# Optimization experiments

Measured on AMD Instinct MI355X. Metric: run time of the kernel, lower is better.

## Reference

```python
import jax, jax.numpy as jnp
import numpy as np

B, S, D, H, F = 2, 2048, 3072, 32, 8192
DH = D // H  # 96
EPS = 1e-5


def setup_inputs() -> dict:
    key = jax.random.key(0)
    ks = jax.random.split(key, 16)
    sd = 0.02
    inp = {
        "hidden_states": jax.random.normal(ks[0], (B, S, D), jnp.float32),
        "ln1_g": jnp.ones((D,), jnp.float32),
        "ln1_b": jnp.zeros((D,), jnp.float32),
        "Wq": jax.random.normal(ks[1], (D, H, DH), jnp.float32) * sd,
        "bq": jnp.zeros((H, DH), jnp.float32),
        "Wk": jax.random.normal(ks[2], (D, H, DH), jnp.float32) * sd,
        "bk": jnp.zeros((H, DH), jnp.float32),
        "Wv": jax.random.normal(ks[3], (D, H, DH), jnp.float32) * sd,
        "bv": jnp.zeros((H, DH), jnp.float32),
        "Wo": jax.random.normal(ks[4], (H, DH, D), jnp.float32) * sd,
        "bo": jnp.zeros((D,), jnp.float32),
        "ln2_g": jnp.ones((D,), jnp.float32),
        "ln2_b": jnp.zeros((D,), jnp.float32),
        "W1": jax.random.normal(ks[5], (D, F), jnp.float32) * sd,
        "b1": jnp.zeros((F,), jnp.float32),
        "W2": jax.random.normal(ks[6], (F, D), jnp.float32) * sd,
        "b2": jnp.zeros((D,), jnp.float32),
    }
    return inp


def _layernorm(x, g, b):
    m = jnp.mean(x, axis=-1, keepdims=True)
    v = jnp.mean(jnp.square(x - m), axis=-1, keepdims=True)
    return (x - m) * jax.lax.rsqrt(v + EPS) * g + b


def reference(hidden_states, ln1_g, ln1_b, Wq, bq, Wk, bk, Wv, bv, Wo, bo,
              ln2_g, ln2_b, W1, b1, W2, b2):
    # --- LN + self-attention + residual ---
    h = _layernorm(hidden_states, ln1_g, ln1_b)  # [B,S,D]
    q = jnp.einsum('bsd,dhk->bshk', h, Wq) + bq  # [B,S,H,DH]
    k = jnp.einsum('bsd,dhk->bshk', h, Wk) + bk
    v = jnp.einsum('bsd,dhk->bshk', h, Wv) + bv
    scale = 1.0 / np.sqrt(DH).astype(np.float32)
    scores = jnp.einsum('bshk,bthk->bhst', q, k) * scale  # [B,H,S,S]
    attn = jax.nn.softmax(scores, axis=-1)
    ctx = jnp.einsum('bhst,bthk->bshk', attn, v)  # [B,S,H,DH]
    attn_out = jnp.einsum('bshk,hkd->bsd', ctx, Wo) + bo
    h1 = hidden_states + attn_out
    # --- LN + MLP + residual ---
    h2 = _layernorm(h1, ln2_g, ln2_b)
    mlp = jax.nn.gelu(h2 @ W1 + b1, approximate=False) @ W2 + b2
    return h1 + mlp
```

## Files before the change

### kernel.cpp

```cpp
#include <hip/hip_runtime.h>
#include <math.h>

#define DEV __device__ __forceinline__

typedef __attribute__((ext_vector_type(8))) __bf16 bfrag;
typedef __attribute__((ext_vector_type(4))) float f4;
typedef __attribute__((ext_vector_type(8))) unsigned short u16x8;
typedef __attribute__((ext_vector_type(4))) unsigned short u16x4;

DEV unsigned short f2bf(float f) {
  unsigned u = __float_as_uint(f);
  u += 0x7fff + ((u >> 16) & 1);
  return (unsigned short)(u >> 16);
}

DEV void gload_lds16(const void* g, void* l) {
  __builtin_amdgcn_global_load_lds((const __attribute__((address_space(1))) void*)g,
                                   (__attribute__((address_space(3))) void*)l, 16, 0, 0);
}

template<int EPI, int OUTBF, int BIASROW>
__global__ __launch_bounds__(256, 2)
void gemm_bt(const unsigned short* __restrict__ A,
             const unsigned short* __restrict__ Bt,
             const float* __restrict__ bias,
             const float* __restrict__ res,
             void* __restrict__ outp,
             int M, int N, int K, int gm, int cm, int cn)
{
  __shared__ unsigned short As[2][128 * 32];
  __shared__ unsigned short Bs[2][128 * 32];
  const int tid = threadIdx.x;
  const int lane = tid & 63;
  const int wid = tid >> 6;
  const int wr = wid >> 1, wc = wid & 1;
  const int l15 = lane & 15, lg = lane >> 4;

  const int xcd = blockIdx.x & 7, bidx = blockIdx.x >> 3;
  const int cgm = gm / cm;
  const int tm = (xcd % cgm) * cm + bidx % cm;
  const int tn = (xcd / cgm) * cn + bidx / cm;
  const long tM = (long)tm * 128;
  const long tN = (long)tn * 128;

  const int c0 = tid, c1 = tid + 256;
  const int r0 = c0 >> 2, k0 = (c0 & 3) * 8;
  const int r1 = c1 >> 2, k1 = (c1 & 3) * 8;

  const unsigned short* A0 = A + (tM + r0) * (long)K + k0;
  const unsigned short* A1 = A + (tM + r1) * (long)K + k1;
  const unsigned short* B0 = Bt + (tN + r0) * (long)K + k0;
  const unsigned short* B1 = Bt + (tN + r1) * (long)K + k1;

  auto stage = [&](int kt, int buf) {
    const long ko = (long)kt * 32;
    gload_lds16(A0 + ko, &As[buf][c0 * 8]);
    gload_lds16(A1 + ko, &As[buf][c1 * 8]);
    gload_lds16(B0 + ko, &Bs[buf][c0 * 8]);
    gload_lds16(B1 + ko, &Bs[buf][c1 * 8]);
  };

  stage(0, 0);
  f4 acc[4][4] = {};
  const int nk = K >> 5;
  int cur = 0;
  __syncthreads();
  for (int kt = 0; kt < nk; ++kt) {
    if (kt + 1 < nk) stage(kt + 1, cur ^ 1);
    bfrag aF[4], bF[4];
#pragma unroll
    for (int m = 0; m < 4; ++m)
      aF[m] = *(const bfrag*)&As[cur][(wr * 64 + m * 16 + l15) * 32 + lg * 8];
#pragma unroll
    for (int n = 0; n < 4; ++n)
      bF[n] = *(const bfrag*)&Bs[cur][(wc * 64 + n * 16 + l15) * 32 + lg * 8];
#pragma unroll
    for (int m = 0; m < 4; ++m)
#pragma unroll
      for (int n = 0; n < 4; ++n)
        acc[m][n] = __builtin_amdgcn_mfma_f32_16x16x32_bf16(aF[m], bF[n], acc[m][n], 0, 0, 0);
    __syncthreads();
    cur ^= 1;
  }

#pragma unroll
  for (int m = 0; m < 4; ++m) {
#pragma unroll
    for (int n = 0; n < 4; ++n) {
      const long col = tN + wc * 64 + n * 16 + l15;
      const float bcol = BIASROW ? 0.f : bias[col];
#pragma unroll
      for (int e = 0; e < 4; ++e) {
        const long row = tM + wr * 64 + m * 16 + lg * 4 + e;
        float v = acc[m][n][e] + (BIASROW ? bias[row] : bcol);
        if constexpr (EPI == 1) v = 0.5f * v * (1.0f + erff(v * 0.70710678118654752f));
        if constexpr (EPI == 2) v += res[row * N + col];
        if constexpr (OUTBF) ((unsigned short*)outp)[row * N + col] = f2bf(v);
        else                 ((float*)outp)[row * N + col] = v;
      }
    }
  }
}

template<int EPI, int OUTBF, int BIASROW>
__global__ __launch_bounds__(512, 2)
void gemm256(const unsigned short* __restrict__ A,
             const unsigned short* __restrict__ Bt,
             const float* __restrict__ bias,
             const float* __restrict__ res,
             void* __restrict__ outp,
             int M, int N, int K, int gm, int cm, int cn)
{
  __shared__ unsigned short As[2][256 * 64];
  __shared__ unsigned short Bs[2][256 * 64];

  const int tid = threadIdx.x;
  const int lane = tid & 63;
  const int wid = tid >> 6;
  const int wm = wid >> 2, wn = wid & 3;
  const int l15 = lane & 15, lg = lane >> 4;

  const int xcd = blockIdx.x & 7, bidx = blockIdx.x >> 3;
  const int cgm = gm / cm;
  const int tm = (xcd % cgm) * cm + bidx % cm;
  const int tn = (xcd / cgm) * cn + bidx / cm;
  const long tM = (long)tm * 256, tN = (long)tn * 256;

  const int srow = tid >> 3;
  const int lslot = (tid & 7) ^ (srow & 7);
  const unsigned short* aSrc = A + (tM + srow) * (long)K + lslot * 8;
  const unsigned short* bSrc = Bt + (tN + srow) * (long)K + lslot * 8;
  const int NT = K >> 6;

  auto stA = [&](int t, int j) {
    gload_lds16(aSrc + (long)t * 64 + (long)j * 64 * K, &As[t & 1][j * 4096 + tid * 8]);
  };
  auto stB = [&](int t, int j) {
    gload_lds16(bSrc + (long)t * 64 + (long)j * 64 * K, &Bs[t & 1][j * 4096 + tid * 8]);
  };

#pragma unroll
  for (int j = 0; j < 4; ++j) stA(0, j);
#pragma unroll
  for (int j = 0; j < 4; ++j) stB(0, j);
  stA(1, 0); stA(1, 2);
#pragma unroll
  for (int j = 0; j < 4; ++j) stB(1, j);
  asm volatile("s_waitcnt vmcnt(6)" ::: "memory");
  __builtin_amdgcn_s_barrier();

  const int aRow = (wm * 128 + l15) * 64;
  const int bRow = (wn * 64 + l15) * 64;
  const int sx = l15 & 7;
  const int sl0 = ((0 + lg) ^ sx) * 8;
  const int sl1 = ((4 + lg) ^ sx) * 8;

  bfrag aF[4][2], bF[4][2];
  f4 acc[8][4] = {};

  int cur = 0;
  for (int t = 0; t < NT; ++t, cur ^= 1) {
    const unsigned short* Ac = As[cur];
    const unsigned short* Bc = Bs[cur];
    const bool s1 = (t + 1 < NT);
    const bool s2 = (t + 2 < NT);

#pragma unroll
    for (int m = 0; m < 4; ++m) {
      aF[m][0] = *(const bfrag*)&Ac[aRow + m * 1024 + sl0];
      aF[m][1] = *(const bfrag*)&Ac[aRow + m * 1024 + sl1];
    }
#pragma unroll
    for (int n = 0; n < 2; ++n) {
      bF[n][0] = *(const bfrag*)&Bc[bRow + n * 1024 + sl0];
      bF[n][1] = *(const bfrag*)&Bc[bRow + n * 1024 + sl1];
    }
    if (s1) { stA(t + 1, 1); stA(t + 1, 3); }
    __builtin_amdgcn_s_barrier();
    asm volatile("s_waitcnt lgkmcnt(0)" ::: "memory");
    __builtin_amdgcn_s_setprio(1);
#pragma unroll
    for (int m = 0; m < 4; ++m)
#pragma unroll
      for (int n = 0; n < 2; ++n) {
        acc[m][n] = __builtin_amdgcn_mfma_f32_16x16x32_bf16(aF[m][0], bF[n][0], acc[m][n], 0, 0, 0);
        acc[m][n] = __builtin_amdgcn_mfma_f32_16x16x32_bf16(aF[m][1], bF[n][1], acc[m][n], 0, 0, 0);
      }
    __builtin_amdgcn_s_setprio(0);
    __builtin_amdgcn_s_barrier();

#pragma unroll
    for (int n = 2; n < 4; ++n) {
      bF[n][0] = *(const bfrag*)&Bc[bRow + n * 1024 + sl0];
      bF[n][1] = *(const bfrag*)&Bc[bRow + n * 1024 + sl1];
    }
    if (s2) { stA(t + 2, 0); stA(t + 2, 2); }
    __builtin_amdgcn_s_barrier();
    asm volatile("s_waitcnt lgkmcnt(0)" ::: "memory");
    __builtin_amdgcn_s_setprio(1);
#pragma unroll
    for (int m = 0; m < 4; ++m)
#pragma unroll
      for (int n = 2; n < 4; ++n) {
        acc[m][n] = __builtin_amdgcn_mfma_f32_16x16x32_bf16(aF[m][0], bF[n][0], acc[m][n], 0, 0, 0);
        acc[m][n] = __builtin_amdgcn_mfma_f32_16x16x32_bf16(aF[m][1], bF[n][1], acc[m][n], 0, 0, 0);
      }
    __builtin_amdgcn_s_setprio(0);
    __builtin_amdgcn_s_barrier();

#pragma unroll
    for (int m = 0; m < 4; ++m) {
      aF[m][0] = *(const bfrag*)&Ac[aRow + 4096 + m * 1024 + sl0];
      aF[m][1] = *(const bfrag*)&Ac[aRow + 4096 + m * 1024 + sl1];
    }
    if (s2) { stB(t + 2, 0); stB(t + 2, 1); }
    __builtin_amdgcn_s_barrier();
    asm volatile("s_waitcnt lgkmcnt(0)" ::: "memory");
    __builtin_amdgcn_s_setprio(1);
#pragma unroll
    for (int m = 0; m < 4; ++m)
#pragma unroll
      for (int n = 0; n < 2; ++n) {
        acc[4 + m][n] = __builtin_amdgcn_mfma_f32_16x16x32_bf16(aF[m][0], bF[n][0], acc[4 + m][n], 0, 0, 0);
        acc[4 + m][n] = __builtin_amdgcn_mfma_f32_16x16x32_bf16(aF[m][1], bF[n][1], acc[4 + m][n], 0, 0, 0);
      }
    __builtin_amdgcn_s_setprio(0);
    __builtin_amdgcn_s_barrier();

    if (s2) { stB(t + 2, 2); stB(t + 2, 3); }
    __builtin_amdgcn_s_setprio(1);
#pragma unroll
    for (int m = 0; m < 4; ++m)
#pragma unroll
      for (int n = 2; n < 4; ++n) {
        acc[4 + m][n] = __builtin_amdgcn_mfma_f32_16x16x32_bf16(aF[m][0], bF[n][0], acc[4 + m][n], 0, 0, 0);
        acc[4 + m][n] = __builtin_amdgcn_mfma_f32_16x16x32_bf16(aF[m][1], bF[n][1], acc[4 + m][n], 0, 0, 0);
      }
    __builtin_amdgcn_s_setprio(0);
    if (s2)      asm volatile("s_waitcnt vmcnt(6)" ::: "memory");
    else if (s1) asm volatile("s_waitcnt vmcnt(0)" ::: "memory");
    __builtin_amdgcn_s_barrier();
  }

#pragma unroll
  for (int m = 0; m < 8; ++m) {
    const long row0 = tM + wm * 128 + m * 16 + lg * 4;
#pragma unroll
    for (int n = 0; n < 4; ++n) {
      const long col = tN + wn * 64 + n * 16 + l15;
      const float bc = BIASROW ? 0.f : bias[col];
#pragma unroll
      for (int e = 0; e < 4; ++e) {
        const long row = row0 + e;
        float v = acc[m][n][e] + (BIASROW ? bias[row] : bc);
        if constexpr (EPI == 1) v = 0.5f * v * (1.0f + erff(v * 0.70710678118654752f));
        if constexpr (EPI == 2) v += res[row * N + col];
        if constexpr (OUTBF) ((unsigned short*)outp)[row * N + col] = f2bf(v);
        else                 ((float*)outp)[row * N + col] = v;
      }
    }
  }
}

__global__ __launch_bounds__(256)
void ln_bf16(const float* __restrict__ x, const float* __restrict__ g,
             const float* __restrict__ b, unsigned short* __restrict__ out)
{
  __shared__ float red[4];
  const int tid = threadIdx.x;
  const long row = blockIdx.x;
  const float* xr = x + row * 3072;
  float4 v[3];
  float s = 0.f;
#pragma unroll
  for (int i = 0; i < 3; ++i) {
    v[i] = *(const float4*)&xr[i * 1024 + tid * 4];
    s += v[i].x + v[i].y + v[i].z + v[i].w;
  }
#pragma unroll
  for (int o = 32; o > 0; o >>= 1) s += __shfl_xor(s, o);
  if ((tid & 63) == 0) red[tid >> 6] = s;
  __syncthreads();
  s = red[0] + red[1] + red[2] + red[3];
  const float mean = s * (1.f / 3072.f);
  float vs = 0.f;
#pragma unroll
  for (int i = 0; i < 3; ++i) {
    const float dx = v[i].x - mean, dy = v[i].y - mean;
    const float dz = v[i].z - mean, dw = v[i].w - mean;
    vs += dx * dx + dy * dy + dz * dz + dw * dw;
  }
#pragma unroll
  for (int o = 32; o > 0; o >>= 1) vs += __shfl_xor(vs, o);
  __syncthreads();
  if ((tid & 63) == 0) red[tid >> 6] = vs;
  __syncthreads();
  vs = red[0] + red[1] + red[2] + red[3];
  const float rstd = rsqrtf(vs * (1.f / 3072.f) + 1e-5f);
#pragma unroll
  for (int i = 0; i < 3; ++i) {
    const int idx = i * 1024 + tid * 4;
    const float* vp = (const float*)&v[i];
    u16x4 o4;
#pragma unroll
    for (int c = 0; c < 4; ++c)
      o4[c] = f2bf((vp[c] - mean) * rstd * g[idx + c] + b[idx + c]);
    *(u16x4*)&out[row * 3072 + idx] = o4;
  }
}

__global__ __launch_bounds__(256)
void prep_weights(const float* __restrict__ Wq, const float* __restrict__ Wk,
                  const float* __restrict__ Wv, const float* __restrict__ Wo,
                  const float* __restrict__ W1, const float* __restrict__ W2,
                  const float* __restrict__ bq, const float* __restrict__ bk,
                  unsigned short* __restrict__ WqkT, unsigned short* __restrict__ WvT,
                  unsigned short* __restrict__ WoT, unsigned short* __restrict__ W1T,
                  unsigned short* __restrict__ W2T, float* __restrict__ bqk)
{
  __shared__ float tile[32][33];
  int bid = blockIdx.x;
  if (bid < 24) {
    const int i = bid * 256 + threadIdx.x;
    bqk[i] = (i < 3072) ? bq[i] : bk[i - 3072];
    return;
  }
  bid -= 24;
  const float* in; unsigned short* out; int R, C, nbx;
  if (bid < 9216)        { in = Wq; out = WqkT;                R = 3072; C = 3072; nbx = 96; }
  else if (bid < 18432)  { in = Wk; out = WqkT + 3072 * 3072;  R = 3072; C = 3072; nbx = 96; bid -= 9216; }
  else if (bid < 27648)  { in = Wv; out = WvT;                 R = 3072; C = 3072; nbx = 96; bid -= 18432; }
  else if (bid < 36864)  { in = Wo; out = WoT;                 R = 3072; C = 3072; nbx = 96; bid -= 27648; }
  else if (bid < 61440)  { in = W1; out = W1T;                 R = 3072; C = 8192; nbx = 256; bid -= 36864; }
  else                   { in = W2; out = W2T;                 R = 8192; C = 3072; nbx = 96; bid -= 61440; }
  const int bx = bid % nbx, by = bid / nbx;
  const int tx = threadIdx.x & 31, ty = threadIdx.x >> 5;
  const long r0 = (long)by * 32, cc0 = (long)bx * 32;
#pragma unroll
  for (int i = 0; i < 4; ++i)
    tile[ty + 8 * i][tx] = in[(r0 + ty + 8 * i) * C + cc0 + tx];
  __syncthreads();
#pragma unroll
  for (int i = 0; i < 4; ++i)
    out[(cc0 + ty + 8 * i) * R + r0 + tx] = f2bf(tile[tx][ty + 8 * i]);
}

__global__ __launch_bounds__(256, 3)
void attn_fwd(const unsigned short* __restrict__ qk,
              const unsigned short* __restrict__ vT,
              unsigned short* __restrict__ ctx)
{
  __shared__ unsigned short Qs[64 * 104];
  __shared__ unsigned short Ks[64 * 104];
  __shared__ unsigned short Vt[96 * 72];
  __shared__ unsigned short Ps[4 * 16 * 72];
  const int tid = threadIdx.x;
  const int lane = tid & 63;
  const int w = tid >> 6;
  const int l15 = lane & 15, lg = lane >> 4;
  const int bid = (blockIdx.x & 7) * 256 + (blockIdx.x >> 3);
  const int qb = bid & 31;
  const int h = (bid >> 5) & 31;
  const int b = bid >> 10;
  const long qkbase = ((long)b * 2048) * 6144 + h * 96;
  const long obase  = ((long)b * 2048) * 3072 + h * 96;
  const long vbase  = (long)(h * 96) * 4096 + (long)b * 2048;
  const int qbase = qb * 64;

#pragma unroll
  for (int i = 0; i < 3; ++i) {
    const int c = tid + i * 256;
    const int r = c / 12, c8 = (c % 12) * 8;
    *(u16x8*)&Qs[r * 104 + c8] = *(const u16x8*)&qk[qkbase + (long)(qbase + r) * 6144 + c8];
  }

  float m_run = -1e30f, l_run = 0.f;
  f4 O[6] = {};
  const float sc = 0.1020620726f * 1.4426950409f;

  for (int t = 0; t < 32; ++t) {
    __syncthreads();
    const int kb = t * 64;
#pragma unroll
    for (int i = 0; i < 3; ++i) {
      const int c = tid + i * 256;
      const int r = c / 12, c8 = (c % 12) * 8;
      *(u16x8*)&Ks[r * 104 + c8] = *(const u16x8*)&qk[qkbase + 3072 + (long)(kb + r) * 6144 + c8];
    }
#pragma unroll
    for (int i = 0; i < 3; ++i) {
      const int idx = tid + i * 256;
      const int d = idx >> 3, c8 = (idx & 7) * 8;
      *(u16x8*)&Vt[d * 72 + c8] = *(const u16x8*)&vT[vbase + (long)d * 4096 + kb + c8];
    }
    __syncthreads();

    f4 sf[4];
#pragma unroll
    for (int mb = 0; mb < 4; ++mb) {
      f4 z = {0.f, 0.f, 0.f, 0.f};
      sf[mb] = z;
#pragma unroll
      for (int ks = 0; ks < 3; ++ks) {
        bfrag kf = *(const bfrag*)&Ks[(mb * 16 + l15) * 104 + ks * 32 + lg * 8];
        bfrag qf = *(const bfrag*)&Qs[(w * 16 + l15) * 104 + ks * 32 + lg * 8];
        sf[mb] = __builtin_amdgcn_mfma_f32_16x16x32_bf16(kf, qf, sf[mb], 0, 0, 0);
      }
    }
    float p[16];
    float tmax = -1e30f;
#pragma unroll
    for (int mb = 0; mb < 4; ++mb)
#pragma unroll
      for (int e = 0; e < 4; ++e) {
        const float sv = sf[mb][e] * sc;
        p[mb * 4 + e] = sv;
        tmax = fmaxf(tmax, sv);
      }
    tmax = fmaxf(tmax, __shfl_xor(tmax, 16));
    tmax = fmaxf(tmax, __shfl_xor(tmax, 32));
    const float mnew = fmaxf(m_run, tmax);
    const float alpha = exp2f(m_run - mnew);
    float psum = 0.f;
#pragma unroll
    for (int i = 0; i < 16; ++i) {
      p[i] = exp2f(p[i] - mnew);
      psum += p[i];
    }
    psum += __shfl_xor(psum, 16);
    psum += __shfl_xor(psum, 32);
    l_run = l_run * alpha + psum;
    m_run = mnew;
#pragma unroll
    for (int mb = 0; mb < 4; ++mb) {
      u16x4 pw;
#pragma unroll
      for (int e = 0; e < 4; ++e) pw[e] = f2bf(p[mb * 4 + e]);
      *(u16x4*)&Ps[w * 1152 + l15 * 72 + mb * 16 + lg * 4] = pw;
    }
    float aE[4];
#pragma unroll
    for (int e = 0; e < 4; ++e) aE[e] = __shfl(alpha, lg * 4 + e);
#pragma unroll
    for (int nb = 0; nb < 6; ++nb)
#pragma unroll
      for (int e = 0; e < 4; ++e) O[nb][e] *= aE[e];
#pragma unroll
    for (int nb = 0; nb < 6; ++nb)
#pragma unroll
      for (int ks = 0; ks < 2; ++ks) {
        bfrag pf = *(const bfrag*)&Ps[w * 1152 + l15 * 72 + ks * 32 + lg * 8];
        bfrag vf = *(const bfrag*)&Vt[(nb * 16 + l15) * 72 + ks * 32 + lg * 8];
        O[nb] = __builtin_amdgcn_mfma_f32_16x16x32_bf16(pf, vf, O[nb], 0, 0, 0);
      }
  }
  float lE[4];
#pragma unroll
  for (int e = 0; e < 4; ++e) lE[e] = 1.f / __shfl(l_run, lg * 4 + e);
#pragma unroll
  for (int nb = 0; nb < 6; ++nb)
#pragma unroll
    for (int e = 0; e < 4; ++e) {
      const long row = qbase + w * 16 + lg * 4 + e;
      ctx[obase + row * 3072 + nb * 16 + l15] = f2bf(O[nb][e] * lE[e]);
    }
}

extern "C" void kernel_launch(void* const* d_in, const int* in_sizes, int n_in,
                              void* d_out, int out_size, void* d_ws, size_t ws_size,
                              hipStream_t stream)
{
  (void)in_sizes; (void)n_in; (void)out_size; (void)ws_size;
  const float* x    = (const float*)d_in[0];
  const float* ln1g = (const float*)d_in[1];
  const float* ln1b = (const float*)d_in[2];
  const float* Wq   = (const float*)d_in[3];
  const float* bq   = (const float*)d_in[4];
  const float* Wk   = (const float*)d_in[5];
  const float* bk   = (const float*)d_in[6];
  const float* Wv   = (const float*)d_in[7];
  const float* bv   = (const float*)d_in[8];
  const float* Wo   = (const float*)d_in[9];
  const float* bo   = (const float*)d_in[10];
  const float* ln2g = (const float*)d_in[11];
  const float* ln2b = (const float*)d_in[12];
  const float* W1   = (const float*)d_in[13];
  const float* b1   = (const float*)d_in[14];
  const float* W2   = (const float*)d_in[15];
  const float* b2   = (const float*)d_in[16];

  char* ws = (char*)d_ws;
  unsigned short* WqkT = (unsigned short*)(ws + 0);
  unsigned short* WvT  = (unsigned short*)(ws + 37748736);
  unsigned short* WoT  = (unsigned short*)(ws + 56623104);
  unsigned short* W1T  = (unsigned short*)(ws + 75497472);
  unsigned short* W2T  = (unsigned short*)(ws + 125829120);
  float*          bqk  = (float*)(ws + 176160768);
  unsigned short* hbf  = (unsigned short*)(ws + 176185344);
  unsigned short* ctxb = hbf;
  unsigned short* qkb  = (unsigned short*)(ws + 201351168);
  unsigned short* h2   = qkb;
  unsigned short* act  = (unsigned short*)(ws + 251682816);
  unsigned short* vTb  = (unsigned short*)(ws + 318791680);
  float*          h1   = (float*)d_out;

  const dim3 blk(256);
  const dim3 blk512(512);

  prep_weights<<<24 + 86016, blk, 0, stream>>>(Wq, Wk, Wv, Wo, W1, W2, bq, bk,
                                               WqkT, WvT, WoT, W1T, W2T, bqk);

  ln_bf16<<<4096, blk, 0, stream>>>(x, ln1g, ln1b, hbf);

  gemm256<0, 1, 0><<<384, blk512, 0, stream>>>(hbf, WqkT, bqk, nullptr, qkb, 4096, 6144, 3072, 16, 8, 6);
  gemm256<0, 1, 1><<<192, blk512, 0, stream>>>(WvT, hbf, bv, nullptr, vTb, 3072, 4096, 3072, 12, 6, 4);

  attn_fwd<<<2048, blk, 0, stream>>>(qkb, vTb, ctxb);

  gemm256<2, 0, 0><<<192, blk512, 0, stream>>>(ctxb, WoT, bo, x, h1, 4096, 3072, 3072, 16, 4, 6);

  ln_bf16<<<4096, blk, 0, stream>>>(h1, ln2g, ln2b, h2);

  gemm256<1, 1, 0><<<512, blk512, 0, stream>>>(h2, W1T, b1, nullptr, act, 4096, 8192, 3072, 16, 8, 8);
  gemm_bt<2, 0, 0><<<768, blk, 0, stream>>>(act, W2T, b2, h1, (float*)d_out, 4096, 3072, 8192, 32, 16, 6);
}
```

Baseline: 1.214 ms.

## Keep Q in registers, prefetch K via registers, load V directly from global

The attention kernel no longer stages Q and V in shared memory. Q fragments are loaded once into registers. The next K tile is prefetched into registers while the current one is consumed, and V fragments are read straight from global memory for each tile, with one barrier per iteration moved to the end of the loop. The goal is less LDS traffic and fewer barriers, with global K loads overlapping compute, at the cost of more registers and redundant uncoalesced V global reads (each wave reads all of V separately).

```diff
diff --git a/kernel.cpp b/kernel.cpp
--- a/kernel.cpp
+++ b/kernel.cpp
@@ -350,9 +350,7 @@
               const unsigned short* __restrict__ vT,
               unsigned short* __restrict__ ctx)
 {
-  __shared__ unsigned short Qs[64 * 104];
   __shared__ unsigned short Ks[64 * 104];
-  __shared__ unsigned short Vt[96 * 72];
   __shared__ unsigned short Ps[4 * 16 * 72];
   const int tid = threadIdx.x;
   const int lane = tid & 63;
@@ -367,33 +365,36 @@
   const long vbase  = (long)(h * 96) * 4096 + (long)b * 2048;
   const int qbase = qb * 64;
 
-#pragma unroll
-  for (int i = 0; i < 3; ++i) {
-    const int c = tid + i * 256;
-    const int r = c / 12, c8 = (c % 12) * 8;
-    *(u16x8*)&Qs[r * 104 + c8] = *(const u16x8*)&qk[qkbase + (long)(qbase + r) * 6144 + c8];
-  }
+  bfrag qf[3];
+#pragma unroll
+  for (int ks = 0; ks < 3; ++ks)
+    qf[ks] = *(const bfrag*)&qk[qkbase + (long)(qbase + w * 16 + l15) * 6144 + ks * 32 + lg * 8];
+
+  const int kc0 = tid, kc1 = tid + 256, kc2 = tid + 512;
+  const int kr0 = kc0 / 12, kk0 = (kc0 % 12) * 8;
+  const int kr1 = kc1 / 12, kk1 = (kc1 % 12) * 8;
+  const int kr2 = kc2 / 12, kk2 = (kc2 % 12) * 8;
+  const unsigned short* kgbase = qk + qkbase + 3072;
+
+  u16x8 kreg0 = *(const u16x8*)&kgbase[(long)kr0 * 6144 + kk0];
+  u16x8 kreg1 = *(const u16x8*)&kgbase[(long)kr1 * 6144 + kk1];
+  u16x8 kreg2 = *(const u16x8*)&kgbase[(long)kr2 * 6144 + kk2];
 
   float m_run = -1e30f, l_run = 0.f;
   f4 O[6] = {};
   const float sc = 0.1020620726f * 1.4426950409f;
 
   for (int t = 0; t < 32; ++t) {
+    *(u16x8*)&Ks[kr0 * 104 + kk0] = kreg0;
+    *(u16x8*)&Ks[kr1 * 104 + kk1] = kreg1;
+    *(u16x8*)&Ks[kr2 * 104 + kk2] = kreg2;
     __syncthreads();
-    const int kb = t * 64;
-#pragma unroll
-    for (int i = 0; i < 3; ++i) {
-      const int c = tid + i * 256;
-      const int r = c / 12, c8 = (c % 12) * 8;
-      *(u16x8*)&Ks[r * 104 + c8] = *(const u16x8*)&qk[qkbase + 3072 + (long)(kb + r) * 6144 + c8];
-    }
-#pragma unroll
-    for (int i = 0; i < 3; ++i) {
-      const int idx = tid + i * 256;
-      const int d = idx >> 3, c8 = (idx & 7) * 8;
-      *(u16x8*)&Vt[d * 72 + c8] = *(const u16x8*)&vT[vbase + (long)d * 4096 + kb + c8];
-    }
-    __syncthreads();
+    if (t + 1 < 32) {
+      const long nb_ = (long)(t + 1) * 64 * 6144;
+      kreg0 = *(const u16x8*)&kgbase[nb_ + (long)kr0 * 6144 + kk0];
+      kreg1 = *(const u16x8*)&kgbase[nb_ + (long)kr1 * 6144 + kk1];
+      kreg2 = *(const u16x8*)&kgbase[nb_ + (long)kr2 * 6144 + kk2];
+    }
 
     f4 sf[4];
 #pragma unroll
@@ -403,8 +404,7 @@
 #pragma unroll
       for (int ks = 0; ks < 3; ++ks) {
         bfrag kf = *(const bfrag*)&Ks[(mb * 16 + l15) * 104 + ks * 32 + lg * 8];
-        bfrag qf = *(const bfrag*)&Qs[(w * 16 + l15) * 104 + ks * 32 + lg * 8];
-        sf[mb] = __builtin_amdgcn_mfma_f32_16x16x32_bf16(kf, qf, sf[mb], 0, 0, 0);
+        sf[mb] = __builtin_amdgcn_mfma_f32_16x16x32_bf16(kf, qf[ks], sf[mb], 0, 0, 0);
       }
     }
     float p[16];
@@ -445,14 +445,24 @@
     for (int nb = 0; nb < 6; ++nb)
 #pragma unroll
       for (int e = 0; e < 4; ++e) O[nb][e] *= aE[e];
+
+    const long vkb = vbase + (long)t * 64;
+    bfrag vf[6][2];
 #pragma unroll
     for (int nb = 0; nb < 6; ++nb)
 #pragma unroll
-      for (int ks = 0; ks < 2; ++ks) {
-        bfrag pf = *(const bfrag*)&Ps[w * 1152 + l15 * 72 + ks * 32 + lg * 8];
-        bfrag vf = *(const bfrag*)&Vt[(nb * 16 + l15) * 72 + ks * 32 + lg * 8];
-        O[nb] = __builtin_amdgcn_mfma_f32_16x16x32_bf16(pf, vf, O[nb], 0, 0, 0);
-      }
+      for (int ks = 0; ks < 2; ++ks)
+        vf[nb][ks] = *(const bfrag*)&vT[vkb + (long)(nb * 16 + l15) * 4096 + ks * 32 + lg * 8];
+    bfrag pf[2];
+#pragma unroll
+    for (int ks = 0; ks < 2; ++ks)
+      pf[ks] = *(const bfrag*)&Ps[w * 1152 + l15 * 72 + ks * 32 + lg * 8];
+#pragma unroll
+    for (int nb = 0; nb < 6; ++nb)
+#pragma unroll
+      for (int ks = 0; ks < 2; ++ks)
+        O[nb] = __builtin_amdgcn_mfma_f32_16x16x32_bf16(pf[ks], vf[nb][ks], O[nb], 0, 0, 0);
+    __syncthreads();
   }
   float lE[4];
 #pragma unroll
```

Result: slower. 1.358 ms (+11.8%).
